# Optimization experiments

Measured on AMD Instinct MI355X. Metric: run time of the kernel, lower is better.

## Reference

```python
import jax, jax.numpy as jnp
import numpy as np

EMBED_DIM = 1024
B, T = 8, 2048


def setup_inputs() -> dict:
    key = jax.random.key(0)
    kx, kw, kb = jax.random.split(key, 3)
    x = jax.random.normal(kx, (B, T, EMBED_DIM), dtype=jnp.float32)
    # nn.Linear(embed_dim, 3*embed_dim): weight [3E, E], bias [3E]
    bound = 1.0 / np.sqrt(EMBED_DIM)
    W = jax.random.uniform(kw, (3 * EMBED_DIM, EMBED_DIM), minval=-bound, maxval=bound, dtype=jnp.float32)
    b = jax.random.uniform(kb, (3 * EMBED_DIM,), minval=-bound, maxval=bound, dtype=jnp.float32)
    return {"x": x, "W": W, "b": b}


def reference(x, W, b):
    E = x.shape[-1]
    qkv = jnp.einsum('bte,fe->btf', x, W) + b            # [B,T,3E]
    q, k, v = jnp.split(qkv, 3, axis=-1)                 # each [B,T,E]
    scale = 1.0 / jnp.sqrt(jnp.asarray(E, dtype=x.dtype))
    scores = jnp.einsum('bqe,bke->bqk', q, k) * scale    # [B,T,T]
    Tq = x.shape[1]
    causal = jnp.tril(jnp.ones((Tq, Tq), dtype=bool))
    scores = jnp.where(causal[None, :, :], scores, jnp.asarray(-jnp.inf, dtype=x.dtype))
    attn = jax.nn.softmax(scores, axis=-1)
    y = jnp.einsum('bqk,bke->bqe', attn, v)              # [B,T,E]
    return y
```

## Files before the change

kernel.cpp:

```cpp
#include <hip/hip_runtime.h>

typedef unsigned short u16;
typedef unsigned int u32;
typedef __attribute__((ext_vector_type(4))) float f32x4;
typedef __attribute__((ext_vector_type(8))) short bf16x8;

#define T_DIM 2048
#define E_DIM 1024
#define NBATCH 8
#define BK 32
#define BUF 32768
#define CORE_LDS (3 * BUF)
#define BUFP 24576
#define COREP_LDS (3 * BUFP)

struct alignas(8)  U16x4 { u16 x, y, z, w; };
struct alignas(16) F32x4 { float x, y, z, w; };

__device__ __forceinline__ u16 f2bf(float f) {
  u32 u = __float_as_uint(f);
  u += 0x7FFFu + ((u >> 16) & 1u);
  return (u16)(u >> 16);
}

__device__ __forceinline__ void gld16(u16* lds, const u16* g) {
  __builtin_amdgcn_global_load_lds((const __attribute__((address_space(1))) void*)g,
                                   (__attribute__((address_space(3))) void*)lds, 16, 0, 0);
}

__device__ __forceinline__ u32 swz7(u32 x) { return x ^ (((x >> 7) & 7u) << 4); }

__device__ __forceinline__ int xcd_swz(int orig, int nwg) {
  int q = nwg >> 3, r = nwg & 7;
  int x = orig & 7, l = orig >> 3;
  return (x < r ? x * (q + 1) : r * (q + 1) + (x - r) * q) + l;
}

#define LGKM0_PIN() do { asm volatile("s_waitcnt lgkmcnt(0)" ::: "memory"); \
                         __builtin_amdgcn_sched_barrier(0); } while (0)

__device__ __forceinline__ void gemm256(const u16* __restrict__ A, const u16* __restrict__ B,
                                        int lda, int ldb, int nK, char* lds0, f32x4 acc[8][4])
{
  const int tid = threadIdx.x, lane = tid & 63, wave = tid >> 6;
  const int wr = wave >> 2, wc = wave & 3;

  const u16* sAp[2]; const u16* sBp[2];
#pragma unroll
  for (int c = 0; c < 2; ++c) {
    u32 L = (u32)(c * 8192 + tid * 16);
    u32 g = swz7(L);
    sAp[c] = A + (size_t)(g >> 6) * lda + ((g & 63u) >> 1);
    sBp[c] = B + (size_t)(g >> 6) * ldb + ((g & 63u) >> 1);
  }
  const u32 doff = (u32)tid * 16u;

  auto stageA = [&](char* buf, int t) {
#pragma unroll
    for (int c = 0; c < 2; ++c)
      gld16((u16*)(buf + c * 8192 + doff), sAp[c] + t * BK);
  };
  auto stageB = [&](char* buf, int t) {
#pragma unroll
    for (int c = 0; c < 2; ++c)
      gld16((u16*)(buf + 16384 + c * 8192 + doff), sBp[c] + t * BK);
  };

  const u32 cb = (u32)(lane >> 4) * 16u;
  u32 aoff[8], boff[4];
#pragma unroll
  for (int m = 0; m < 8; ++m)
    aoff[m] = swz7((u32)(wr * 128 + m * 16 + (lane & 15)) * 64u + cb);
#pragma unroll
  for (int n = 0; n < 4; ++n)
    boff[n] = 16384u + swz7((u32)(wc * 64 + n * 16 + (lane & 15)) * 64u + cb);

  stageA(lds0, 0); stageB(lds0, 0);
  stageA(lds0 + BUF, 1); stageB(lds0 + BUF, 1);

  int bc = 0;
  bf16x8 a[4], b[4];
  for (int t = 0; t < nK; ++t) {
    char* bufR = lds0 + bc * BUF;
    int b2 = bc + 2; if (b2 >= 3) b2 -= 3;
    char* bufW = lds0 + b2 * BUF;

    if (t + 1 < nK) asm volatile("s_waitcnt vmcnt(4)" ::: "memory");
    else            asm volatile("s_waitcnt vmcnt(0)" ::: "memory");
    __builtin_amdgcn_s_barrier();
    __builtin_amdgcn_sched_barrier(0);

    if (t + 2 < nK) stageA(bufW, t + 2);
#pragma unroll
    for (int j = 0; j < 4; ++j) a[j] = *(const bf16x8*)(bufR + aoff[j]);
#pragma unroll
    for (int n = 0; n < 4; ++n) b[n] = *(const bf16x8*)(bufR + boff[n]);
    LGKM0_PIN();
    __builtin_amdgcn_s_setprio(1);
#pragma unroll
    for (int j = 0; j < 4; ++j)
#pragma unroll
      for (int n = 0; n < 4; ++n)
        acc[j][n] = __builtin_amdgcn_mfma_f32_16x16x32_bf16(a[j], b[n], acc[j][n], 0, 0, 0);
    __builtin_amdgcn_s_setprio(0);
    __builtin_amdgcn_sched_barrier(0);

    if (t + 2 < nK) stageB(bufW, t + 2);
#pragma unroll
    for (int j = 0; j < 4; ++j) a[j] = *(const bf16x8*)(bufR + aoff[4 + j]);
    LGKM0_PIN();
    __builtin_amdgcn_s_setprio(1);
#pragma unroll
    for (int j = 0; j < 4; ++j)
#pragma unroll
      for (int n = 0; n < 4; ++n)
        acc[4 + j][n] = __builtin_amdgcn_mfma_f32_16x16x32_bf16(a[j], b[n], acc[4 + j][n], 0, 0, 0);
    __builtin_amdgcn_s_setprio(0);
    __builtin_amdgcn_sched_barrier(0);

    bc = bc + 1 == 3 ? 0 : bc + 1;
  }
}

__device__ __forceinline__ void gemm128n(const u16* __restrict__ A, const u16* __restrict__ B,
                                         int lda, int ldb, int nK, char* lds0, f32x4 acc[4][4])
{
  const int tid = threadIdx.x, lane = tid & 63, wave = tid >> 6;
  const int wr = wave >> 2, wc = wave & 3;

  const u16* sA0; const u16* sBp[2];
  {
    u32 g = swz7((u32)tid * 16u);
    sA0 = A + (size_t)(g >> 6) * lda + ((g & 63u) >> 1);
  }
#pragma unroll
  for (int c = 0; c < 2; ++c) {
    u32 g = swz7((u32)(c * 8192 + tid * 16));
    sBp[c] = B + (size_t)(g >> 6) * ldb + ((g & 63u) >> 1);
  }
  const u32 doff = (u32)tid * 16u;

  auto stageA = [&](char* buf, int t) {
    gld16((u16*)(buf + doff), sA0 + t * BK);
  };
  auto stageB = [&](char* buf, int t) {
#pragma unroll
    for (int c = 0; c < 2; ++c)
      gld16((u16*)(buf + 8192 + c * 8192 + doff), sBp[c] + t * BK);
  };

  const u32 cb = (u32)(lane >> 4) * 16u;
  u32 aoff[4], boff[4];
#pragma unroll
  for (int m = 0; m < 4; ++m)
    aoff[m] = swz7((u32)(wr * 64 + m * 16 + (lane & 15)) * 64u + cb);
#pragma unroll
  for (int n = 0; n < 4; ++n)
    boff[n] = 8192u + swz7((u32)(wc * 64 + n * 16 + (lane & 15)) * 64u + cb);

  stageA(lds0, 0); stageB(lds0, 0);
  stageA(lds0 + BUFP, 1); stageB(lds0 + BUFP, 1);

  int bc = 0;
  bf16x8 a[2], b[4];
  for (int t = 0; t < nK; ++t) {
    char* bufR = lds0 + bc * BUFP;
    int b2 = bc + 2; if (b2 >= 3) b2 -= 3;
    char* bufW = lds0 + b2 * BUFP;

    if (t + 1 < nK) asm volatile("s_waitcnt vmcnt(3)" ::: "memory");
    else            asm volatile("s_waitcnt vmcnt(0)" ::: "memory");
    __builtin_amdgcn_s_barrier();
    __builtin_amdgcn_sched_barrier(0);

    if (t + 2 < nK) stageA(bufW, t + 2);
    a[0] = *(const bf16x8*)(bufR + aoff[0]);
    a[1] = *(const bf16x8*)(bufR + aoff[1]);
#pragma unroll
    for (int n = 0; n < 4; ++n) b[n] = *(const bf16x8*)(bufR + boff[n]);
    LGKM0_PIN();
    __builtin_amdgcn_s_setprio(1);
#pragma unroll
    for (int j = 0; j < 2; ++j)
#pragma unroll
      for (int n = 0; n < 4; ++n)
        acc[j][n] = __builtin_amdgcn_mfma_f32_16x16x32_bf16(a[j], b[n], acc[j][n], 0, 0, 0);
    __builtin_amdgcn_s_setprio(0);
    __builtin_amdgcn_sched_barrier(0);

    if (t + 2 < nK) stageB(bufW, t + 2);
    a[0] = *(const bf16x8*)(bufR + aoff[2]);
    a[1] = *(const bf16x8*)(bufR + aoff[3]);
    LGKM0_PIN();
    __builtin_amdgcn_s_setprio(1);
#pragma unroll
    for (int j = 0; j < 2; ++j)
#pragma unroll
      for (int n = 0; n < 4; ++n)
        acc[2 + j][n] = __builtin_amdgcn_mfma_f32_16x16x32_bf16(a[j], b[n], acc[2 + j][n], 0, 0, 0);
    __builtin_amdgcn_s_setprio(0);
    __builtin_amdgcn_sched_barrier(0);

    bc = bc + 1 == 3 ? 0 : bc + 1;
  }
}

__global__ __launch_bounds__(256) void k_cvt(const float* __restrict__ in, u16* __restrict__ out, int n4)
{
  int i = blockIdx.x * 256 + threadIdx.x;
  if (i >= n4) return;
  F32x4 v = *(const F32x4*)&in[(size_t)i * 4];
  U16x4 o;
  o.x = f2bf(v.x); o.y = f2bf(v.y); o.z = f2bf(v.z); o.w = f2bf(v.w);
  *(U16x4*)&out[(size_t)i * 4] = o;
}

__global__ __launch_bounds__(512, 2) void k_qkv(const u16* __restrict__ Xb, const u16* __restrict__ Wb,
                                                const float* __restrict__ bias,
                                                u16* __restrict__ Q, u16* __restrict__ Kmat,
                                                u16* __restrict__ Vt)
{
  __shared__ __align__(16) char lds[CORE_LDS];
  const int wg = xcd_swz(blockIdx.x, gridDim.x);
  const int my = wg / 12, nx = wg % 12;
  const int m0 = my * 256, n0 = nx * 256;
  const int tid = threadIdx.x, lane = tid & 63, wave = tid >> 6;
  const int wr = wave >> 2, wc = wave & 3;
  f32x4 acc[8][4] = {};
  gemm256(Xb + (size_t)m0 * E_DIM, Wb + (size_t)n0 * E_DIM, E_DIM, E_DIM, E_DIM / BK, lds, acc);
  __syncthreads();

  char* wsl = lds + wave * 8192;
  const int region = nx >> 2;
  const int nlb = (n0 & (E_DIM - 1)) + wc * 64;

  if (region < 2) {
    u16* dst = region ? Kmat : Q;
#pragma unroll
    for (int p = 0; p < 2; ++p) {
#pragma unroll
      for (int n = 0; n < 4; ++n) {
        const float bn = bias[n0 + wc * 64 + n * 16 + (lane & 15)];
#pragma unroll
        for (int mm = 0; mm < 4; ++mm)
#pragma unroll
          for (int r = 0; r < 4; ++r) {
            const int rl = mm * 16 + ((lane >> 4) << 2) + r;
            const int cl = n * 16 + (lane & 15);
            u32 byte = (u32)(rl * 128 + cl * 2) ^ (u32)((rl & 7) << 4);
            *(u16*)(wsl + byte) = f2bf(acc[p * 4 + mm][n][r] + bn);
          }
      }
      asm volatile("s_waitcnt lgkmcnt(0)" ::: "memory");
      const int rowb = m0 + wr * 128 + p * 64;
#pragma unroll
      for (int it = 0; it < 8; ++it) {
        const int rl = it * 8 + (lane >> 3);
        const int c16 = lane & 7;
        u32 byte = (u32)(rl * 128 + c16 * 16) ^ (u32)((rl & 7) << 4);
        bf16x8 v = *(const bf16x8*)(wsl + byte);
        *(bf16x8*)&dst[(size_t)(rowb + rl) * E_DIM + nlb + c16 * 8] = v;
      }
      if (p == 0) asm volatile("s_waitcnt lgkmcnt(0)" ::: "memory");
    }
  } else {
    const int bl = m0 >> 11;
    const int tb = (m0 & (T_DIM - 1)) + wr * 128;
#pragma unroll
    for (int p = 0; p < 2; ++p) {
#pragma unroll
      for (int n = 0; n < 4; ++n) {
        const float bn = bias[n0 + wc * 64 + n * 16 + (lane & 15)];
        const int e_l = n * 16 + (lane & 15);
#pragma unroll
        for (int mm = 0; mm < 4; ++mm)
#pragma unroll
          for (int r = 0; r < 4; ++r) {
            const int tl = mm * 16 + ((lane >> 4) << 2) + r;
            u32 byte = (u32)(e_l * 128 + tl * 2) ^ (u32)((e_l & 7) << 4);
            *(u16*)(wsl + byte) = f2bf(acc[p * 4 + mm][n][r] + bn);
          }
      }
      asm volatile("s_waitcnt lgkmcnt(0)" ::: "memory");
#pragma unroll
      for (int it = 0; it < 8; ++it) {
        const int e_l = it * 8 + (lane >> 3);
        const int t16 = lane & 7;
        u32 byte = (u32)(e_l * 128 + t16 * 16) ^ (u32)((e_l & 7) << 4);
        bf16x8 v = *(const bf16x8*)(wsl + byte);
        *(bf16x8*)&Vt[((size_t)bl * E_DIM + nlb + e_l) * T_DIM + tb + p * 64 + t16 * 8] = v;
      }
      if (p == 0) asm volatile("s_waitcnt lgkmcnt(0)" ::: "memory");
    }
  }
}

__global__ __launch_bounds__(512, 2) void k_sp(const u16* __restrict__ Q, const u16* __restrict__ Kmat,
                                               u16* __restrict__ P, float* __restrict__ lc)
{
  __shared__ __align__(16) char lds[CORE_LDS];
  const int wg = xcd_swz(blockIdx.x, gridDim.x);
  const int b = wg / 36;
  const int ti = wg % 36;
  int iq = 0;
  while ((iq + 1) * (iq + 2) / 2 <= ti) ++iq;
  const int ik = ti - iq * (iq + 1) / 2;
  const int tid = threadIdx.x, lane = tid & 63, wave = tid >> 6;
  const int wr = wave >> 2, wc = wave & 3;
  f32x4 acc[8][4] = {};
  const u16* Qp = Q    + (size_t)b * T_DIM * E_DIM + (size_t)iq * 256 * E_DIM;
  const u16* Kp = Kmat + (size_t)b * T_DIM * E_DIM + (size_t)ik * 256 * E_DIM;
  gemm256(Qp, Kp, E_DIM, E_DIM, E_DIM / BK, lds, acc);
  __syncthreads();

  const float scale = 0.03125f;
  if (ik == iq) {
#pragma unroll
    for (int n = 0; n < 4; ++n) {
      const int kg = wc * 64 + n * 16 + (lane & 15);
#pragma unroll
      for (int m = 0; m < 8; ++m) {
        const int qg0 = wr * 128 + m * 16 + ((lane >> 4) << 2);
#pragma unroll
        for (int r = 0; r < 4; ++r)
          acc[m][n][r] = (kg > qg0 + r) ? 0.f
                        : __expf(fminf(acc[m][n][r] * scale, 60.f));
      }
    }
  } else {
#pragma unroll
    for (int m = 0; m < 8; ++m)
#pragma unroll
      for (int n = 0; n < 4; ++n)
#pragma unroll
        for (int r = 0; r < 4; ++r)
          acc[m][n][r] = __expf(fminf(acc[m][n][r] * scale, 60.f));
  }

  float* red2 = (float*)lds;
  float Ls[8][4];
#pragma unroll
  for (int m = 0; m < 8; ++m)
#pragma unroll
    for (int r = 0; r < 4; ++r) {
      float s = acc[m][0][r] + acc[m][1][r] + acc[m][2][r] + acc[m][3][r];
#pragma unroll
      for (int off = 1; off <= 8; off <<= 1) s += __shfl_xor(s, off, 64);
      Ls[m][r] = s;
    }
  if ((lane & 15) == 0) {
#pragma unroll
    for (int m = 0; m < 8; ++m)
#pragma unroll
      for (int r = 0; r < 4; ++r)
        red2[wc * 256 + wr * 128 + m * 16 + ((lane >> 4) << 2) + r] = Ls[m][r];
  }
  __syncthreads();
  if (wc == 0 && (lane & 15) == 0) {
#pragma unroll
    for (int m = 0; m < 8; ++m)
#pragma unroll
      for (int r = 0; r < 4; ++r) {
        const int row = wr * 128 + m * 16 + ((lane >> 4) << 2) + r;
        const float l = red2[row] + red2[256 + row] + red2[512 + row] + red2[768 + row];
        lc[((size_t)b * T_DIM + iq * 256 + row) * 8 + ik] = l;
      }
  }
  __syncthreads();

  u16* Pb = P + (size_t)b * T_DIM * T_DIM;
  char* wsl = lds + 16384 + wave * 8192;
#pragma unroll
  for (int p = 0; p < 2; ++p) {
#pragma unroll
    for (int n = 0; n < 4; ++n)
#pragma unroll
      for (int mm = 0; mm < 4; ++mm)
#pragma unroll
        for (int r = 0; r < 4; ++r) {
          const int rl = mm * 16 + ((lane >> 4) << 2) + r;
          const int cl = n * 16 + (lane & 15);
          u32 byte = (u32)(rl * 128 + cl * 2) ^ (u32)((rl & 7) << 4);
          *(u16*)(wsl + byte) = f2bf(acc[p * 4 + mm][n][r]);
        }
    asm volatile("s_waitcnt lgkmcnt(0)" ::: "memory");
    const int rowb = iq * 256 + wr * 128 + p * 64;
    const int colb = ik * 256 + wc * 64;
#pragma unroll
    for (int it = 0; it < 8; ++it) {
      const int rl = it * 8 + (lane >> 3);
      const int c16 = lane & 7;
      u32 byte = (u32)(rl * 128 + c16 * 16) ^ (u32)((rl & 7) << 4);
      bf16x8 v = *(const bf16x8*)(wsl + byte);
      *(bf16x8*)&Pb[(size_t)(rowb + rl) * T_DIM + colb + c16 * 8] = v;
    }
    if (p == 0) asm volatile("s_waitcnt lgkmcnt(0)" ::: "memory");
  }
}

__global__ __launch_bounds__(256) void k_finish(const float* __restrict__ lc, float* __restrict__ fin)
{
  const int rg = blockIdx.x * 256 + threadIdx.x;
  const int q = rg & (T_DIM - 1);
  const int C = (q >> 8) + 1;
  const float* l = lc + (size_t)rg * 8;
  float L = 0.f;
  for (int c = 0; c < C; ++c) L += l[c];
  fin[rg] = 1.f / L;
}

__global__ __launch_bounds__(512, 2) void k_pv(const u16* __restrict__ P, const u16* __restrict__ Vt,
                                               const float* __restrict__ fin,
                                               float* __restrict__ out, int batch0)
{
  __shared__ __align__(16) char lds[COREP_LDS];
  const int wg = xcd_swz(blockIdx.x, gridDim.x);
  const int bl = wg >> 5, rr = wg & 31;
  const int pr = rr >> 2, ie = rr & 3;
  const int tid = threadIdx.x, lane = tid & 63, wave = tid >> 6;
  const int wr = wave >> 2, wc = wave & 3;

  const u16* Bp = Vt + (size_t)bl * E_DIM * T_DIM + (size_t)ie * 256 * T_DIM;

#pragma unroll
  for (int mem = 0; mem < 2; ++mem) {
    const int iq = mem ? 15 - pr : pr;
    const int nch = (iq >> 1) + 1;

    __syncthreads();
    f32x4 acc[4][4] = {};
    const u16* Ap = P + (size_t)bl * T_DIM * T_DIM + (size_t)iq * 128 * T_DIM;
    gemm128n(Ap, Bp, T_DIM, T_DIM, nch * 8, lds, acc);

#pragma unroll
    for (int m = 0; m < 4; ++m) {
      const int qg0 = iq * 128 + wr * 64 + m * 16 + ((lane >> 4) << 2);
#pragma unroll
      for (int r = 0; r < 4; ++r) {
        const int qg = qg0 + r;
        const float il = fin[bl * T_DIM + qg];
        float* orow = out + ((size_t)(batch0 + bl) * T_DIM + qg) * E_DIM;
#pragma unroll
        for (int n = 0; n < 4; ++n) {
          const int eg = ie * 256 + wc * 64 + n * 16 + (lane & 15);
          orow[eg] = acc[m][n][r] * il;
        }
      }
    }
  }
}

extern "C" void kernel_launch(void* const* d_in, const int* in_sizes, int n_in,
                              void* d_out, int out_size, void* d_ws, size_t ws_size,
                              hipStream_t stream)
{
  const float* x    = (const float*)d_in[0];
  const float* W    = (const float*)d_in[1];
  const float* bias = (const float*)d_in[2];
  float* out = (float*)d_out;

  char* ws = (char*)d_ws;
  const size_t ALIGN = 256;
  auto up = [&](size_t v) { return (v + ALIGN - 1) & ~(ALIGN - 1); };

  const size_t szWb = up((size_t)3 * E_DIM * E_DIM * 2);
  const size_t szX  = up((size_t)T_DIM * E_DIM * 2);
  const size_t szP  = up((size_t)T_DIM * T_DIM * 2);
  const size_t szM  = up((size_t)T_DIM * 8 * 4);
  const size_t szI  = up((size_t)T_DIM * 4);
  const size_t perB = 4 * szX + szP + szM + szI;

  int nb = 1;
  for (int cand = NBATCH; cand >= 1; --cand) {
    if (szWb + (size_t)cand * perB <= ws_size) { nb = cand; break; }
  }

  u16* Wb = (u16*)ws;
  {
    int n4 = 3 * E_DIM * E_DIM / 4;
    k_cvt<<<(n4 + 255) / 256, 256, 0, stream>>>(W, Wb, n4);
  }

  for (int b0 = 0; b0 < NBATCH; b0 += nb) {
    const int nbc = (NBATCH - b0 < nb) ? (NBATCH - b0) : nb;
    size_t o = szWb;
    u16* Xb    = (u16*)(ws + o);   o += (size_t)nbc * szX;
    u16* Qb    = (u16*)(ws + o);   o += (size_t)nbc * szX;
    u16* Kb    = (u16*)(ws + o);   o += (size_t)nbc * szX;
    u16* Vt    = (u16*)(ws + o);   o += (size_t)nbc * szX;
    u16* P     = (u16*)(ws + o);   o += (size_t)nbc * szP;
    float* lcA = (float*)(ws + o); o += (size_t)nbc * szM;
    float* fin = (float*)(ws + o); o += (size_t)nbc * szI;

    {
      int n4 = nbc * T_DIM * E_DIM / 4;
      k_cvt<<<(n4 + 255) / 256, 256, 0, stream>>>(x + (size_t)b0 * T_DIM * E_DIM, Xb, n4);
    }
    k_qkv<<<dim3(96 * nbc), 512, 0, stream>>>(Xb, Wb, bias, Qb, Kb, Vt);
    k_sp<<<dim3(36 * nbc), 512, 0, stream>>>(Qb, Kb, P, lcA);
    k_finish<<<dim3(nbc * T_DIM / 256), 256, 0, stream>>>(lcA, fin);
    k_pv<<<dim3(32 * nbc), 512, 0, stream>>>(P, Vt, fin, out, b0);
  }
}
```

Measured before the change: 246.2 us.

## Shrink QKV and score GEMM tiles to 128x256 for more workgroups

```diff
diff --git a/kernel.cpp b/kernel.cpp
--- a/kernel.cpp
+++ b/kernel.cpp
@@ -9,8 +9,6 @@
 #define E_DIM 1024
 #define NBATCH 8
 #define BK 32
-#define BUF 32768
-#define CORE_LDS (3 * BUF)
 #define BUFP 24576
 #define COREP_LDS (3 * BUFP)
 
@@ -38,89 +36,6 @@
 
 #define LGKM0_PIN() do { asm volatile("s_waitcnt lgkmcnt(0)" ::: "memory"); \
                          __builtin_amdgcn_sched_barrier(0); } while (0)
-
-__device__ __forceinline__ void gemm256(const u16* __restrict__ A, const u16* __restrict__ B,
-                                        int lda, int ldb, int nK, char* lds0, f32x4 acc[8][4])
-{
-  const int tid = threadIdx.x, lane = tid & 63, wave = tid >> 6;
-  const int wr = wave >> 2, wc = wave & 3;
-
-  const u16* sAp[2]; const u16* sBp[2];
-#pragma unroll
-  for (int c = 0; c < 2; ++c) {
-    u32 L = (u32)(c * 8192 + tid * 16);
-    u32 g = swz7(L);
-    sAp[c] = A + (size_t)(g >> 6) * lda + ((g & 63u) >> 1);
-    sBp[c] = B + (size_t)(g >> 6) * ldb + ((g & 63u) >> 1);
-  }
-  const u32 doff = (u32)tid * 16u;
-
-  auto stageA = [&](char* buf, int t) {
-#pragma unroll
-    for (int c = 0; c < 2; ++c)
-      gld16((u16*)(buf + c * 8192 + doff), sAp[c] + t * BK);
-  };
-  auto stageB = [&](char* buf, int t) {
-#pragma unroll
-    for (int c = 0; c < 2; ++c)
-      gld16((u16*)(buf + 16384 + c * 8192 + doff), sBp[c] + t * BK);
-  };
-
-  const u32 cb = (u32)(lane >> 4) * 16u;
-  u32 aoff[8], boff[4];
-#pragma unroll
-  for (int m = 0; m < 8; ++m)
-    aoff[m] = swz7((u32)(wr * 128 + m * 16 + (lane & 15)) * 64u + cb);
-#pragma unroll
-  for (int n = 0; n < 4; ++n)
-    boff[n] = 16384u + swz7((u32)(wc * 64 + n * 16 + (lane & 15)) * 64u + cb);
-
-  stageA(lds0, 0); stageB(lds0, 0);
-  stageA(lds0 + BUF, 1); stageB(lds0 + BUF, 1);
-
-  int bc = 0;
-  bf16x8 a[4], b[4];
-  for (int t = 0; t < nK; ++t) {
-    char* bufR = lds0 + bc * BUF;
-    int b2 = bc + 2; if (b2 >= 3) b2 -= 3;
-    char* bufW = lds0 + b2 * BUF;
-
-    if (t + 1 < nK) asm volatile("s_waitcnt vmcnt(4)" ::: "memory");
-    else            asm volatile("s_waitcnt vmcnt(0)" ::: "memory");
-    __builtin_amdgcn_s_barrier();
-    __builtin_amdgcn_sched_barrier(0);
-
-    if (t + 2 < nK) stageA(bufW, t + 2);
-#pragma unroll
-    for (int j = 0; j < 4; ++j) a[j] = *(const bf16x8*)(bufR + aoff[j]);
-#pragma unroll
-    for (int n = 0; n < 4; ++n) b[n] = *(const bf16x8*)(bufR + boff[n]);
-    LGKM0_PIN();
-    __builtin_amdgcn_s_setprio(1);
-#pragma unroll
-    for (int j = 0; j < 4; ++j)
-#pragma unroll
-      for (int n = 0; n < 4; ++n)
-        acc[j][n] = __builtin_amdgcn_mfma_f32_16x16x32_bf16(a[j], b[n], acc[j][n], 0, 0, 0);
-    __builtin_amdgcn_s_setprio(0);
-    __builtin_amdgcn_sched_barrier(0);
-
-    if (t + 2 < nK) stageB(bufW, t + 2);
-#pragma unroll
-    for (int j = 0; j < 4; ++j) a[j] = *(const bf16x8*)(bufR + aoff[4 + j]);
-    LGKM0_PIN();
-    __builtin_amdgcn_s_setprio(1);
-#pragma unroll
-    for (int j = 0; j < 4; ++j)
-#pragma unroll
-      for (int n = 0; n < 4; ++n)
-        acc[4 + j][n] = __builtin_amdgcn_mfma_f32_16x16x32_bf16(a[j], b[n], acc[4 + j][n], 0, 0, 0);
-    __builtin_amdgcn_s_setprio(0);
-    __builtin_amdgcn_sched_barrier(0);
-
-    bc = bc + 1 == 3 ? 0 : bc + 1;
-  }
-}
 
 __device__ __forceinline__ void gemm128n(const u16* __restrict__ A, const u16* __restrict__ B,
                                          int lda, int ldb, int nK, char* lds0, f32x4 acc[4][4])
@@ -215,186 +130,169 @@
   *(U16x4*)&out[(size_t)i * 4] = o;
 }
 
-__global__ __launch_bounds__(512, 2) void k_qkv(const u16* __restrict__ Xb, const u16* __restrict__ Wb,
+__global__ __launch_bounds__(512, 4) void k_qkv(const u16* __restrict__ Xb, const u16* __restrict__ Wb,
                                                 const float* __restrict__ bias,
                                                 u16* __restrict__ Q, u16* __restrict__ Kmat,
                                                 u16* __restrict__ Vt)
 {
-  __shared__ __align__(16) char lds[CORE_LDS];
+  __shared__ __align__(16) char lds[COREP_LDS];
   const int wg = xcd_swz(blockIdx.x, gridDim.x);
   const int my = wg / 12, nx = wg % 12;
-  const int m0 = my * 256, n0 = nx * 256;
+  const int m0 = my * 128, n0 = nx * 256;
   const int tid = threadIdx.x, lane = tid & 63, wave = tid >> 6;
   const int wr = wave >> 2, wc = wave & 3;
-  f32x4 acc[8][4] = {};
-  gemm256(Xb + (size_t)m0 * E_DIM, Wb + (size_t)n0 * E_DIM, E_DIM, E_DIM, E_DIM / BK, lds, acc);
+  f32x4 acc[4][4] = {};
+  gemm128n(Xb + (size_t)m0 * E_DIM, Wb + (size_t)n0 * E_DIM, E_DIM, E_DIM, E_DIM / BK, lds, acc);
   __syncthreads();
 
   char* wsl = lds + wave * 8192;
   const int region = nx >> 2;
   const int nlb = (n0 & (E_DIM - 1)) + wc * 64;
+  const int g4 = (lane >> 4) << 2;
 
   if (region < 2) {
     u16* dst = region ? Kmat : Q;
 #pragma unroll
-    for (int p = 0; p < 2; ++p) {
-#pragma unroll
-      for (int n = 0; n < 4; ++n) {
-        const float bn = bias[n0 + wc * 64 + n * 16 + (lane & 15)];
-#pragma unroll
-        for (int mm = 0; mm < 4; ++mm)
-#pragma unroll
-          for (int r = 0; r < 4; ++r) {
-            const int rl = mm * 16 + ((lane >> 4) << 2) + r;
-            const int cl = n * 16 + (lane & 15);
-            u32 byte = (u32)(rl * 128 + cl * 2) ^ (u32)((rl & 7) << 4);
-            *(u16*)(wsl + byte) = f2bf(acc[p * 4 + mm][n][r] + bn);
-          }
-      }
-      asm volatile("s_waitcnt lgkmcnt(0)" ::: "memory");
-      const int rowb = m0 + wr * 128 + p * 64;
-#pragma unroll
-      for (int it = 0; it < 8; ++it) {
-        const int rl = it * 8 + (lane >> 3);
-        const int c16 = lane & 7;
-        u32 byte = (u32)(rl * 128 + c16 * 16) ^ (u32)((rl & 7) << 4);
-        bf16x8 v = *(const bf16x8*)(wsl + byte);
-        *(bf16x8*)&dst[(size_t)(rowb + rl) * E_DIM + nlb + c16 * 8] = v;
-      }
-      if (p == 0) asm volatile("s_waitcnt lgkmcnt(0)" ::: "memory");
-    }
-  } else {
-    const int bl = m0 >> 11;
-    const int tb = (m0 & (T_DIM - 1)) + wr * 128;
-#pragma unroll
-    for (int p = 0; p < 2; ++p) {
-#pragma unroll
-      for (int n = 0; n < 4; ++n) {
-        const float bn = bias[n0 + wc * 64 + n * 16 + (lane & 15)];
-        const int e_l = n * 16 + (lane & 15);
-#pragma unroll
-        for (int mm = 0; mm < 4; ++mm)
-#pragma unroll
-          for (int r = 0; r < 4; ++r) {
-            const int tl = mm * 16 + ((lane >> 4) << 2) + r;
-            u32 byte = (u32)(e_l * 128 + tl * 2) ^ (u32)((e_l & 7) << 4);
-            *(u16*)(wsl + byte) = f2bf(acc[p * 4 + mm][n][r] + bn);
-          }
-      }
-      asm volatile("s_waitcnt lgkmcnt(0)" ::: "memory");
-#pragma unroll
-      for (int it = 0; it < 8; ++it) {
-        const int e_l = it * 8 + (lane >> 3);
-        const int t16 = lane & 7;
-        u32 byte = (u32)(e_l * 128 + t16 * 16) ^ (u32)((e_l & 7) << 4);
-        bf16x8 v = *(const bf16x8*)(wsl + byte);
-        *(bf16x8*)&Vt[((size_t)bl * E_DIM + nlb + e_l) * T_DIM + tb + p * 64 + t16 * 8] = v;
-      }
-      if (p == 0) asm volatile("s_waitcnt lgkmcnt(0)" ::: "memory");
-    }
-  }
-}
-
-__global__ __launch_bounds__(512, 2) void k_sp(const u16* __restrict__ Q, const u16* __restrict__ Kmat,
-                                               u16* __restrict__ P, float* __restrict__ lc)
-{
-  __shared__ __align__(16) char lds[CORE_LDS];
-  const int wg = xcd_swz(blockIdx.x, gridDim.x);
-  const int b = wg / 36;
-  const int ti = wg % 36;
-  int iq = 0;
-  while ((iq + 1) * (iq + 2) / 2 <= ti) ++iq;
-  const int ik = ti - iq * (iq + 1) / 2;
-  const int tid = threadIdx.x, lane = tid & 63, wave = tid >> 6;
-  const int wr = wave >> 2, wc = wave & 3;
-  f32x4 acc[8][4] = {};
-  const u16* Qp = Q    + (size_t)b * T_DIM * E_DIM + (size_t)iq * 256 * E_DIM;
-  const u16* Kp = Kmat + (size_t)b * T_DIM * E_DIM + (size_t)ik * 256 * E_DIM;
-  gemm256(Qp, Kp, E_DIM, E_DIM, E_DIM / BK, lds, acc);
-  __syncthreads();
-
-  const float scale = 0.03125f;
-  if (ik == iq) {
-#pragma unroll
     for (int n = 0; n < 4; ++n) {
-      const int kg = wc * 64 + n * 16 + (lane & 15);
-#pragma unroll
-      for (int m = 0; m < 8; ++m) {
-        const int qg0 = wr * 128 + m * 16 + ((lane >> 4) << 2);
-#pragma unroll
-        for (int r = 0; r < 4; ++r)
-          acc[m][n][r] = (kg > qg0 + r) ? 0.f
-                        : __expf(fminf(acc[m][n][r] * scale, 60.f));
-      }
-    }
-  } else {
-#pragma unroll
-    for (int m = 0; m < 8; ++m)
-#pragma unroll
-      for (int n = 0; n < 4; ++n)
-#pragma unroll
-        for (int r = 0; r < 4; ++r)
-          acc[m][n][r] = __expf(fminf(acc[m][n][r] * scale, 60.f));
-  }
-
-  float* red2 = (float*)lds;
-  float Ls[8][4];
-#pragma unroll
-  for (int m = 0; m < 8; ++m)
-#pragma unroll
-    for (int r = 0; r < 4; ++r) {
-      float s = acc[m][0][r] + acc[m][1][r] + acc[m][2][r] + acc[m][3][r];
-#pragma unroll
-      for (int off = 1; off <= 8; off <<= 1) s += __shfl_xor(s, off, 64);
-      Ls[m][r] = s;
-    }
-  if ((lane & 15) == 0) {
-#pragma unroll
-    for (int m = 0; m < 8; ++m)
-#pragma unroll
-      for (int r = 0; r < 4; ++r)
-        red2[wc * 256 + wr * 128 + m * 16 + ((lane >> 4) << 2) + r] = Ls[m][r];
-  }
-  __syncthreads();
-  if (wc == 0 && (lane & 15) == 0) {
-#pragma unroll
-    for (int m = 0; m < 8; ++m)
-#pragma unroll
-      for (int r = 0; r < 4; ++r) {
-        const int row = wr * 128 + m * 16 + ((lane >> 4) << 2) + r;
-        const float l = red2[row] + red2[256 + row] + red2[512 + row] + red2[768 + row];
-        lc[((size_t)b * T_DIM + iq * 256 + row) * 8 + ik] = l;
-      }
-  }
-  __syncthreads();
-
-  u16* Pb = P + (size_t)b * T_DIM * T_DIM;
-  char* wsl = lds + 16384 + wave * 8192;
-#pragma unroll
-  for (int p = 0; p < 2; ++p) {
-#pragma unroll
-    for (int n = 0; n < 4; ++n)
-#pragma unroll
-      for (int mm = 0; mm < 4; ++mm)
+      const float bn = bias[n0 + wc * 64 + n * 16 + (lane & 15)];
+#pragma unroll
+      for (int m = 0; m < 4; ++m)
 #pragma unroll
         for (int r = 0; r < 4; ++r) {
-          const int rl = mm * 16 + ((lane >> 4) << 2) + r;
+          const int rl = m * 16 + g4 + r;
           const int cl = n * 16 + (lane & 15);
           u32 byte = (u32)(rl * 128 + cl * 2) ^ (u32)((rl & 7) << 4);
-          *(u16*)(wsl + byte) = f2bf(acc[p * 4 + mm][n][r]);
+          *(u16*)(wsl + byte) = f2bf(acc[m][n][r] + bn);
         }
+    }
     asm volatile("s_waitcnt lgkmcnt(0)" ::: "memory");
-    const int rowb = iq * 256 + wr * 128 + p * 64;
-    const int colb = ik * 256 + wc * 64;
+    const int rowb = m0 + wr * 64;
 #pragma unroll
     for (int it = 0; it < 8; ++it) {
       const int rl = it * 8 + (lane >> 3);
       const int c16 = lane & 7;
       u32 byte = (u32)(rl * 128 + c16 * 16) ^ (u32)((rl & 7) << 4);
       bf16x8 v = *(const bf16x8*)(wsl + byte);
-      *(bf16x8*)&Pb[(size_t)(rowb + rl) * T_DIM + colb + c16 * 8] = v;
-    }
-    if (p == 0) asm volatile("s_waitcnt lgkmcnt(0)" ::: "memory");
+      *(bf16x8*)&dst[(size_t)(rowb + rl) * E_DIM + nlb + c16 * 8] = v;
+    }
+  } else {
+    const int bl = m0 >> 11;
+    const int tb = (m0 & (T_DIM - 1)) + wr * 64;
+#pragma unroll
+    for (int n = 0; n < 4; ++n) {
+      const float bn = bias[n0 + wc * 64 + n * 16 + (lane & 15)];
+      const int e_l = n * 16 + (lane & 15);
+#pragma unroll
+      for (int m = 0; m < 4; ++m)
+#pragma unroll
+        for (int r = 0; r < 4; ++r) {
+          const int tl = m * 16 + g4 + r;
+          u32 byte = (u32)(e_l * 128 + tl * 2) ^ (u32)((e_l & 7) << 4);
+          *(u16*)(wsl + byte) = f2bf(acc[m][n][r] + bn);
+        }
+    }
+    asm volatile("s_waitcnt lgkmcnt(0)" ::: "memory");
+#pragma unroll
+    for (int it = 0; it < 8; ++it) {
+      const int e_l = it * 8 + (lane >> 3);
+      const int t16 = lane & 7;
+      u32 byte = (u32)(e_l * 128 + t16 * 16) ^ (u32)((e_l & 7) << 4);
+      bf16x8 v = *(const bf16x8*)(wsl + byte);
+      *(bf16x8*)&Vt[((size_t)bl * E_DIM + nlb + e_l) * T_DIM + tb + t16 * 8] = v;
+    }
+  }
+}
+
+__global__ __launch_bounds__(512, 4) void k_sp(const u16* __restrict__ Q, const u16* __restrict__ Kmat,
+                                               u16* __restrict__ P, float* __restrict__ lc)
+{
+  __shared__ __align__(16) char lds[COREP_LDS];
+  const int wg = xcd_swz(blockIdx.x, gridDim.x);
+  const int b = wg / 72;
+  int ti = wg % 72;
+  int iq = 0;
+  while (ti >= (iq >> 1) + 1) { ti -= (iq >> 1) + 1; ++iq; }
+  const int ik = ti;
+  const int tid = threadIdx.x, lane = tid & 63, wave = tid >> 6;
+  const int wr = wave >> 2, wc = wave & 3;
+  const int g4 = (lane >> 4) << 2;
+  f32x4 acc[4][4] = {};
+  const u16* Qp = Q    + (size_t)b * T_DIM * E_DIM + (size_t)iq * 128 * E_DIM;
+  const u16* Kp = Kmat + (size_t)b * T_DIM * E_DIM + (size_t)ik * 256 * E_DIM;
+  gemm128n(Qp, Kp, E_DIM, E_DIM, E_DIM / BK, lds, acc);
+  __syncthreads();
+
+  const float scale = 0.03125f;
+  const bool diag = (ik == (iq >> 1));
+  const int diagoff = iq * 128 - ik * 256;
+#pragma unroll
+  for (int n = 0; n < 4; ++n) {
+    const int cl = wc * 64 + n * 16 + (lane & 15);
+#pragma unroll
+    for (int m = 0; m < 4; ++m) {
+      const int rl0 = wr * 64 + m * 16 + g4;
+#pragma unroll
+      for (int r = 0; r < 4; ++r) {
+        if (diag && cl > diagoff + rl0 + r) acc[m][n][r] = 0.f;
+        else acc[m][n][r] = __expf(fminf(acc[m][n][r] * scale, 60.f));
+      }
+    }
+  }
+
+  float* red2 = (float*)lds;
+  float Ls[4][4];
+#pragma unroll
+  for (int m = 0; m < 4; ++m)
+#pragma unroll
+    for (int r = 0; r < 4; ++r) {
+      float s = acc[m][0][r] + acc[m][1][r] + acc[m][2][r] + acc[m][3][r];
+#pragma unroll
+      for (int off = 1; off <= 8; off <<= 1) s += __shfl_xor(s, off, 64);
+      Ls[m][r] = s;
+    }
+  if ((lane & 15) == 0) {
+#pragma unroll
+    for (int m = 0; m < 4; ++m)
+#pragma unroll
+      for (int r = 0; r < 4; ++r)
+        red2[wc * 128 + wr * 64 + m * 16 + g4 + r] = Ls[m][r];
+  }
+  __syncthreads();
+  if (wc == 0 && (lane & 15) == 0) {
+#pragma unroll
+    for (int m = 0; m < 4; ++m)
+#pragma unroll
+      for (int r = 0; r < 4; ++r) {
+        const int row = wr * 64 + m * 16 + g4 + r;
+        const float l = red2[row] + red2[128 + row] + red2[256 + row] + red2[384 + row];
+        lc[((size_t)b * T_DIM + iq * 128 + row) * 8 + ik] = l;
+      }
+  }
+  __syncthreads();
+
+  u16* Pb = P + (size_t)b * T_DIM * T_DIM;
+  char* wsl = lds + wave * 8192;
+#pragma unroll
+  for (int n = 0; n < 4; ++n)
+#pragma unroll
+    for (int m = 0; m < 4; ++m)
+#pragma unroll
+      for (int r = 0; r < 4; ++r) {
+        const int rl = m * 16 + g4 + r;
+        const int cl = n * 16 + (lane & 15);
+        u32 byte = (u32)(rl * 128 + cl * 2) ^ (u32)((rl & 7) << 4);
+        *(u16*)(wsl + byte) = f2bf(acc[m][n][r]);
+      }
+  asm volatile("s_waitcnt lgkmcnt(0)" ::: "memory");
+  const int rowb = iq * 128 + wr * 64;
+  const int colb = ik * 256 + wc * 64;
+#pragma unroll
+  for (int it = 0; it < 8; ++it) {
+    const int rl = it * 8 + (lane >> 3);
+    const int c16 = lane & 7;
+    u32 byte = (u32)(rl * 128 + c16 * 16) ^ (u32)((rl & 7) << 4);
+    bf16x8 v = *(const bf16x8*)(wsl + byte);
+    *(bf16x8*)&Pb[(size_t)(rowb + rl) * T_DIM + colb + c16 * 8] = v;
   }
 }
 
@@ -496,8 +394,8 @@
       int n4 = nbc * T_DIM * E_DIM / 4;
       k_cvt<<<(n4 + 255) / 256, 256, 0, stream>>>(x + (size_t)b0 * T_DIM * E_DIM, Xb, n4);
     }
-    k_qkv<<<dim3(96 * nbc), 512, 0, stream>>>(Xb, Wb, bias, Qb, Kb, Vt);
-    k_sp<<<dim3(36 * nbc), 512, 0, stream>>>(Qb, Kb, P, lcA);
+    k_qkv<<<dim3(192 * nbc), 512, 0, stream>>>(Xb, Wb, bias, Qb, Kb, Vt);
+    k_sp<<<dim3(72 * nbc), 512, 0, stream>>>(Qb, Kb, P, lcA);
     k_finish<<<dim3(nbc * T_DIM / 256), 256, 0, stream>>>(lcA, fin);
     k_pv<<<dim3(32 * nbc), 512, 0, stream>>>(P, Vt, fin, out, b0);
   }
```

Result: faster. 237.9 us (-3.4%).
